# Kernel optimization log

Hardware: AMD Instinct MI355X
Metric: run time of the kernel (lower is better)

## Reference

```python
import jax, jax.numpy as jnp
import numpy as np

N_NODES = 50000
N_EDGES = 600000
IN_F = 128
OUT_F = 128
SMALL = max(IN_F // 10, 1)  # floor(128/10) = 12
D_K = np.sqrt(SMALL).astype(np.float32)


def setup_inputs() -> dict:
    key = jax.random.key(0)
    ks = jax.random.split(key, 10)
    node_data = jax.random.normal(ks[0], (N_NODES, IN_F), dtype=jnp.float32)
    src = jax.random.randint(ks[1], (N_EDGES,), 0, N_NODES, dtype=jnp.int32)
    dst = jax.random.randint(ks[2], (N_EDGES,), 0, N_NODES, dtype=jnp.int32)
    s_q = 1.0 / np.sqrt(IN_F)
    Wq = jax.random.uniform(ks[3], (SMALL, IN_F), jnp.float32, -s_q, s_q)
    bq = jax.random.uniform(ks[4], (SMALL,), jnp.float32, -s_q, s_q)
    Wk = jax.random.uniform(ks[5], (SMALL, IN_F), jnp.float32, -s_q, s_q)
    bk = jax.random.uniform(ks[6], (SMALL,), jnp.float32, -s_q, s_q)
    W1 = jax.random.uniform(ks[7], (OUT_F, IN_F), jnp.float32, -s_q, s_q)
    W2 = jax.random.uniform(ks[8], (OUT_F, IN_F), jnp.float32, -s_q, s_q)
    b2 = jax.random.uniform(ks[9], (OUT_F,), jnp.float32, -s_q, s_q)
    return {"node_data": node_data, "src": src, "dst": dst,
            "Wq": Wq, "bq": bq, "Wk": Wk, "bk": bk,
            "W1": W1, "W2": W2, "b2": b2}


def reference(node_data, src, dst, Wq, bq, Wk, bk, W1, W2, b2):
    N = node_data.shape[0]
    # dgl.add_self_loop: append (i, i) for every node -> each dst has >= 1 edge
    loops = jnp.arange(N, dtype=src.dtype)
    s = jnp.concatenate([src, loops])
    d = jnp.concatenate([dst, loops])

    # query = Tanh(Linear), key = Linear  (shapes [N, SMALL])
    q = jnp.tanh(node_data @ Wq.T + bq)
    k = node_data @ Wk.T + bk

    # per-edge score: sum(query[src] * key[dst]) / sqrt(small)
    scores = jnp.sum(q[s] * k[d], axis=1) / D_K  # [E]

    # softmax over incoming edges of each dst node (segment softmax)
    seg_max = jax.ops.segment_max(scores, d, num_segments=N)
    w = jnp.exp(scores - seg_max[d])
    seg_sum = jax.ops.segment_sum(w, d, num_segments=N)
    w = w / seg_sum[d]  # [E]

    # weighted scatter-aggregate of src node inputs -> [N, IN_F]
    att = jax.ops.segment_sum(w[:, None] * node_data[s], d, num_segments=N)

    # DeepSetLayer: layer1(node_data) + layer2(node attention)
    x = node_data @ W1.T + (att @ W2.T + b2)
    # per-row L2 ('fro' over dim=1) normalization, then ReLU
    x = x / jnp.linalg.norm(x, axis=1, keepdims=True)
    return jax.nn.relu(x)
```

## Files before the change

### kernel.cpp

```cpp
#include <hip/hip_runtime.h>
#include <hip/hip_bf16.h>
#include <math.h>
#include <stdint.h>


#define IN_F 128
#define SMALL 12
#define QK_PAD 16
#define SCAN_ITEMS 8
#define SCAN_CHUNK 2048

typedef __attribute__((ext_vector_type(8))) short short8;
typedef __attribute__((ext_vector_type(4))) float f32x4;

__device__ __forceinline__ unsigned short f2bf(float f) {
    union { float f; unsigned u; } v; v.f = f;
    unsigned r = v.u + 0x7fff + ((v.u >> 16) & 1);
    return (unsigned short)(r >> 16);
}

__device__ __forceinline__ float2 bf2x2(unsigned v) {
    union { unsigned u; float f; } a, b;
    a.u = v << 16;
    b.u = v & 0xffff0000u;
    return make_float2(a.f, b.f);
}

__device__ __forceinline__ float dot12(const float* __restrict__ qrow,
                                       float4 c0, float4 c1, float4 c2) {
    float4 a = ((const float4*)qrow)[0];
    float4 b = ((const float4*)qrow)[1];
    float4 c = ((const float4*)qrow)[2];
    return a.x*c0.x + a.y*c0.y + a.z*c0.z + a.w*c0.w
         + b.x*c1.x + b.y*c1.y + b.z*c1.z + b.w*c1.w
         + c.x*c2.x + c.y*c2.y + c.z*c2.z + c.w*c2.w;
}

__device__ __forceinline__ short8 ld_bf8(const float* p) {
    float4 x0 = *(const float4*)p;
    float4 x1 = *(const float4*)(p + 4);
    short8 a;
    a[0] = (short)f2bf(x0.x); a[1] = (short)f2bf(x0.y);
    a[2] = (short)f2bf(x0.z); a[3] = (short)f2bf(x0.w);
    a[4] = (short)f2bf(x1.x); a[5] = (short)f2bf(x1.y);
    a[6] = (short)f2bf(x1.z); a[7] = (short)f2bf(x1.w);
    return a;
}

__global__ __launch_bounds__(256) void prep_kernel(
    const float* __restrict__ nd,
    const float* __restrict__ Wq, const float* __restrict__ bq,
    const float* __restrict__ Wk, const float* __restrict__ bk,
    const int* __restrict__ dst,
    const float* __restrict__ W1, const float* __restrict__ W2,
    float* __restrict__ q, float* __restrict__ kf,
    unsigned short* __restrict__ ndb, int* __restrict__ cnt,
    unsigned short* __restrict__ rank, unsigned short* __restrict__ Wc,
    int N, int E, int NBQK, int NBCNT)
{
    int t = threadIdx.x;
    int b = blockIdx.x;

    if (b < NBQK) {
        int wv = t >> 6;
        int lane = t & 63;
        int col = lane & 15;
        int quad = lane >> 4;
        int tbase = b * 64 + wv * 16;

        int arow = tbase + col;
        int rowc = (arow < N) ? arow : (N - 1);
        const float* ap = nd + (size_t)rowc * IN_F + quad * 8;
        unsigned short* np = ndb + (size_t)arow * IN_F + quad * 8;

        const float* w0 = ((col < 12) ? (Wq + (size_t)col * IN_F)
                                      : (Wk + (size_t)(col - 12) * IN_F)) + quad * 8;
        const float* w1 = Wk + (size_t)((col < 8) ? (col + 4) : 4) * IN_F + quad * 8;
        bool hasw1 = (col < 8);

        f32x4 acc0 = (f32x4)0.f, acc1 = (f32x4)0.f;
#pragma unroll
        for (int ks = 0; ks < 4; ks++) {
            int k0 = ks * 32;
            short8 a = ld_bf8(ap + k0);
            if (arow < N) *(short8*)(np + k0) = a;
            short8 bb0 = ld_bf8(w0 + k0);
            short8 bb1 = hasw1 ? ld_bf8(w1 + k0) : (short8)0;
            acc0 = __builtin_amdgcn_mfma_f32_16x16x32_bf16(a, bb0, acc0, 0, 0, 0);
            acc1 = __builtin_amdgcn_mfma_f32_16x16x32_bf16(a, bb1, acc1, 0, 0, 0);
        }
        float bias0 = (col < 12) ? bq[col] : bk[col - 12];
        float bias1 = (col < 8) ? bk[col + 4] : 0.f;
#pragma unroll
        for (int r = 0; r < 4; r++) {
            int node = tbase + quad * 4 + r;
            if (node < N) {
                float v0 = acc0[r] + bias0;
                if (col < 12) q[(size_t)node * QK_PAD + col] = tanhf(v0);
                else          kf[(size_t)node * QK_PAD + (col - 12)] = v0;
                if (hasw1)    kf[(size_t)node * QK_PAD + col + 4] = acc1[r] + bias1;
            }
        }
    } else if (b < NBQK + NBCNT) {
        int ET = E + N;
        int stride = NBCNT * 256;
        for (int i = (b - NBQK) * 256 + t; i < ET; i += stride) {
            int d = (i < E) ? dst[i] : (i - E);
            rank[i] = (unsigned short)atomicAdd(&cnt[d], 1);
        }
    } else {
        int idx = (b - NBQK - NBCNT) * 256 + t;
        int f = idx >> 8, k = idx & 255;
        float v = (k < 128) ? W1[f * 128 + k] : W2[f * 128 + (k - 128)];
        Wc[idx] = f2bf(v);
    }
}

__global__ __launch_bounds__(256) void scan_local_kernel(
    int* __restrict__ off, int* __restrict__ bsum, int N)
{
    __shared__ int tsum[256];
    int t = threadIdx.x;
    int base = blockIdx.x * SCAN_CHUNK + t * SCAN_ITEMS;
    int v[SCAN_ITEMS];
    int s = 0;
#pragma unroll
    for (int i = 0; i < SCAN_ITEMS; i++) {
        int idx = base + i;
        v[i] = (idx < N) ? off[idx] : 0;
        s += v[i];
    }
    tsum[t] = s;
    __syncthreads();
    for (int d = 1; d < 256; d <<= 1) {
        int x = (t >= d) ? tsum[t - d] : 0;
        __syncthreads();
        tsum[t] += x;
        __syncthreads();
    }
    int excl = (t == 0) ? 0 : tsum[t - 1];
#pragma unroll
    for (int i = 0; i < SCAN_ITEMS; i++) {
        int idx = base + i;
        if (idx < N) off[idx] = excl;
        excl += v[i];
    }
    if (t == 255) bsum[blockIdx.x] = tsum[255];
}

__global__ __launch_bounds__(256) void scan_add_kernel(
    int* __restrict__ off, const int* __restrict__ bsum, int N, int NB)
{
    __shared__ int pre2[2];
    int t = threadIdx.x;
    if (t == 0) {
        int p = 0, tot = 0;
        for (int i = 0; i < NB; i++) {
            int v = bsum[i];
            if (i < (int)blockIdx.x) p += v;
            tot += v;
        }
        pre2[0] = p; pre2[1] = tot;
    }
    __syncthreads();
    int add = pre2[0];
    if (blockIdx.x == 0 && t == 0) off[N] = pre2[1];

    int base = blockIdx.x * SCAN_CHUNK + t * SCAN_ITEMS;
#pragma unroll
    for (int i = 0; i < SCAN_ITEMS; i++) {
        int j = base + i;
        if (j < N) off[j] += add;
    }
}

__global__ __launch_bounds__(256) void scatter_kernel(
    const int* __restrict__ src, const int* __restrict__ dst,
    const int* __restrict__ off, const unsigned short* __restrict__ rank,
    unsigned short* __restrict__ esrc, int E, int N)
{
    int i = blockIdx.x * 256 + threadIdx.x;
    if (i >= E + N) return;
    int d, s;
    if (i < E) { d = dst[i]; s = src[i]; }
    else       { d = i - E; s = d; }
    esrc[off[d] + (int)rank[i]] = (unsigned short)s;
}

__global__ __launch_bounds__(256) void attn_kernel(
    const unsigned short* __restrict__ ndb, const float* __restrict__ q,
    const float* __restrict__ kf, const int* __restrict__ off,
    const unsigned short* __restrict__ esrc, float* __restrict__ att, int N)
{
    const float INVDK = 0.28867513459481287f;
    int t = threadIdx.x;
    int lane = t & 63;
    int l16 = lane & 15;
    int gbase = lane & 48;
    int wid = blockIdx.x * 16 + (t >> 4);
    if (wid >= N) return;

    int start = off[wid];
    int deg = off[wid + 1] - start;

    const float4* kp = (const float4*)(kf + (size_t)wid * QK_PAD);
    float4 c0 = kp[0], c1 = kp[1], c2 = kp[2];

    float acc[8];
#pragma unroll
    for (int j = 0; j < 8; j++) acc[j] = 0.f;
    float inv;

    const unsigned short* nb = ndb + l16 * 8;

#define ACCUM(vv, ww) do {                                                    \
        float2 f0 = bf2x2((vv).x), f1 = bf2x2((vv).y);                        \
        float2 f2 = bf2x2((vv).z), f3 = bf2x2((vv).w);                        \
        acc[0] += (ww) * f0.x; acc[1] += (ww) * f0.y;                         \
        acc[2] += (ww) * f1.x; acc[3] += (ww) * f1.y;                         \
        acc[4] += (ww) * f2.x; acc[5] += (ww) * f2.y;                         \
        acc[6] += (ww) * f3.x; acc[7] += (ww) * f3.y;                         \
    } while (0)

    if (deg <= 16) {
        float sc = -INFINITY;
        int si = 0;
        if (l16 < deg) {
            si = (int)esrc[start + l16];
            sc = dot12(q + (size_t)si * QK_PAD, c0, c1, c2) * INVDK;
        }
        float m = sc;
#pragma unroll
        for (int o = 8; o > 0; o >>= 1) m = fmaxf(m, __shfl_xor(m, o));
        float w = (l16 < deg) ? __expf(sc - m) : 0.f;
        float ls = w;
#pragma unroll
        for (int o = 8; o > 0; o >>= 1) ls += __shfl_xor(ls, o);
        inv = 1.f / ls;

        int i = 0;
        for (; i + 4 <= deg; i += 4) {
            float w0 = __shfl(w, gbase | i);       int r0 = __shfl(si, gbase | i);
            float w1 = __shfl(w, gbase | (i + 1)); int r1 = __shfl(si, gbase | (i + 1));
            float w2 = __shfl(w, gbase | (i + 2)); int r2 = __shfl(si, gbase | (i + 2));
            float w3 = __shfl(w, gbase | (i + 3)); int r3 = __shfl(si, gbase | (i + 3));
            uint4 v0 = *(const uint4*)(nb + (size_t)r0 * IN_F);
            uint4 v1 = *(const uint4*)(nb + (size_t)r1 * IN_F);
            uint4 v2 = *(const uint4*)(nb + (size_t)r2 * IN_F);
            uint4 v3 = *(const uint4*)(nb + (size_t)r3 * IN_F);
            ACCUM(v0, w0); ACCUM(v1, w1); ACCUM(v2, w2); ACCUM(v3, w3);
        }
        for (; i < deg; i++) {
            float wi = __shfl(w, gbase | i);
            int ri = __shfl(si, gbase | i);
            uint4 v = *(const uint4*)(nb + (size_t)ri * IN_F);
            ACCUM(v, wi);
        }
    } else {
        float m = -INFINITY;
        for (int i = l16; i < deg; i += 16) {
            int s2 = (int)esrc[start + i];
            m = fmaxf(m, dot12(q + (size_t)s2 * QK_PAD, c0, c1, c2) * INVDK);
        }
#pragma unroll
        for (int o = 8; o > 0; o >>= 1) m = fmaxf(m, __shfl_xor(m, o));
        float ls = 0.f;
        for (int i = l16; i < deg; i += 16) {
            int s2 = (int)esrc[start + i];
            ls += __expf(dot12(q + (size_t)s2 * QK_PAD, c0, c1, c2) * INVDK - m);
        }
#pragma unroll
        for (int o = 8; o > 0; o >>= 1) ls += __shfl_xor(ls, o);
        inv = 1.f / ls;

        for (int base2 = 0; base2 < deg; base2 += 16) {
            int cnt2 = deg - base2; if (cnt2 > 16) cnt2 = 16;
            float w = 0.f; int si = 0;
            if (l16 < cnt2) {
                si = (int)esrc[start + base2 + l16];
                w = __expf(dot12(q + (size_t)si * QK_PAD, c0, c1, c2) * INVDK - m);
            }
            int i = 0;
            for (; i + 4 <= cnt2; i += 4) {
                float w0 = __shfl(w, gbase | i);       int r0 = __shfl(si, gbase | i);
                float w1 = __shfl(w, gbase | (i + 1)); int r1 = __shfl(si, gbase | (i + 1));
                float w2 = __shfl(w, gbase | (i + 2)); int r2 = __shfl(si, gbase | (i + 2));
                float w3 = __shfl(w, gbase | (i + 3)); int r3 = __shfl(si, gbase | (i + 3));
                uint4 v0 = *(const uint4*)(nb + (size_t)r0 * IN_F);
                uint4 v1 = *(const uint4*)(nb + (size_t)r1 * IN_F);
                uint4 v2 = *(const uint4*)(nb + (size_t)r2 * IN_F);
                uint4 v3 = *(const uint4*)(nb + (size_t)r3 * IN_F);
                ACCUM(v0, w0); ACCUM(v1, w1); ACCUM(v2, w2); ACCUM(v3, w3);
            }
            for (; i < cnt2; i++) {
                float wi = __shfl(w, gbase | i);
                int ri = __shfl(si, gbase | i);
                uint4 v = *(const uint4*)(nb + (size_t)ri * IN_F);
                ACCUM(v, wi);
            }
        }
    }
#undef ACCUM

    float* op = att + (size_t)wid * IN_F + l16 * 8;
    float4 s0, s1;
    s0.x = acc[0] * inv; s0.y = acc[1] * inv; s0.z = acc[2] * inv; s0.w = acc[3] * inv;
    s1.x = acc[4] * inv; s1.y = acc[5] * inv; s1.z = acc[6] * inv; s1.w = acc[7] * inv;
    *(float4*)op = s0;
    *(float4*)(op + 4) = s1;
}

__global__ __launch_bounds__(256) void final_kernel(
    const unsigned short* __restrict__ ndb, const float* __restrict__ nd,
    const float* __restrict__ att,
    const unsigned short* __restrict__ Wc, const float* __restrict__ b2,
    float* __restrict__ out, int N)
{
    int wv = threadIdx.x >> 6;
    int lane = threadIdx.x & 63;
    int col = lane & 15;
    int quad = lane >> 4;

    int arow = blockIdx.x * 64 + wv * 16 + col;
    int rowc = (arow < N) ? arow : (N - 1);
    const unsigned short* a0p = ndb + (size_t)rowc * IN_F + quad * 8;
    const float* a1p = ((arow < N) ? att : nd) + (size_t)rowc * IN_F + quad * 8;

    f32x4 acc[8];
#pragma unroll
    for (int i = 0; i < 8; i++) acc[i] = (f32x4)0.f;

#pragma unroll
    for (int ks = 0; ks < 8; ks++) {
        int k0 = ks * 32;
        short8 a;
        if (ks < 4) a = *(const short8*)(a0p + k0);
        else        a = ld_bf8(a1p + (k0 - 128));
#pragma unroll
        for (int ft = 0; ft < 8; ft++) {
            int n = ft * 16 + col;
            short8 bb = *(const short8*)(Wc + (size_t)n * 256 + k0 + quad * 8);
            acc[ft] = __builtin_amdgcn_mfma_f32_16x16x32_bf16(a, bb, acc[ft], 0, 0, 0);
        }
    }

    float bias[8];
#pragma unroll
    for (int ft = 0; ft < 8; ft++) bias[ft] = b2[ft * 16 + col];

#pragma unroll
    for (int r = 0; r < 4; r++) {
        int node = blockIdx.x * 64 + wv * 16 + quad * 4 + r;
        float v[8];
        float ps = 0.f;
#pragma unroll
        for (int ft = 0; ft < 8; ft++) {
            v[ft] = acc[ft][r] + bias[ft];
            ps += v[ft] * v[ft];
        }
        ps += __shfl_xor(ps, 1);
        ps += __shfl_xor(ps, 2);
        ps += __shfl_xor(ps, 4);
        ps += __shfl_xor(ps, 8);
        float rn = rsqrtf(ps);
        if (node < N) {
            float* op = out + (size_t)node * 128 + col;
#pragma unroll
            for (int ft = 0; ft < 8; ft++)
                op[ft * 16] = fmaxf(v[ft] * rn, 0.f);
        }
    }
}

static inline char* align_up(char* p, size_t a) {
    return (char*)(((uintptr_t)p + (a - 1)) & ~(uintptr_t)(a - 1));
}

extern "C" void kernel_launch(void* const* d_in, const int* in_sizes, int n_in,
                              void* d_out, int out_size, void* d_ws, size_t ws_size,
                              hipStream_t stream) {
    const float* node_data = (const float*)d_in[0];
    const int*   src       = (const int*)d_in[1];
    const int*   dst       = (const int*)d_in[2];
    const float* Wq        = (const float*)d_in[3];
    const float* bq        = (const float*)d_in[4];
    const float* Wk        = (const float*)d_in[5];
    const float* bk        = (const float*)d_in[6];
    const float* W1        = (const float*)d_in[7];
    const float* W2        = (const float*)d_in[8];
    const float* b2        = (const float*)d_in[9];
    float* out = (float*)d_out;

    int N = in_sizes[0] / IN_F;
    int E = in_sizes[1];
    int ET = E + N;
    int NB = (N + SCAN_CHUNK - 1) / SCAN_CHUNK;
    int NBQK = (N + 63) / 64;
    int NBCNT = 512;
    int NBCVT = 128;

    char* w = (char*)d_ws;
    float* q  = (float*)w;  w += (size_t)N * QK_PAD * sizeof(float);
    float* kf = (float*)w;  w += (size_t)N * QK_PAD * sizeof(float);
    w = align_up(w, 256);
    unsigned short* ndb = (unsigned short*)w;  w += (size_t)N * IN_F * sizeof(unsigned short);
    w = align_up(w, 256);
    unsigned short* Wc = (unsigned short*)w;  w += 128 * 256 * sizeof(unsigned short);
    int* off  = (int*)w;  w += (size_t)(N + 1) * sizeof(int);
    int* bsum = (int*)w;  w += 256 * sizeof(int);
    unsigned short* rank = (unsigned short*)w;  w += (size_t)ET * sizeof(unsigned short);
    w = align_up(w, 256);
    unsigned short* esrc = (unsigned short*)w;  w += (size_t)ET * sizeof(unsigned short);
    float* att = out;

    hipMemsetAsync(off, 0, (size_t)(N + 1) * sizeof(int), stream);

    prep_kernel<<<NBQK + NBCNT + NBCVT, 256, 0, stream>>>(
        node_data, Wq, bq, Wk, bk, dst, W1, W2,
        q, kf, ndb, off, rank, Wc, N, E, NBQK, NBCNT);
    scan_local_kernel<<<NB, 256, 0, stream>>>(off, bsum, N);
    scan_add_kernel<<<NB, 256, 0, stream>>>(off, bsum, N, NB);
    scatter_kernel<<<(ET + 255) / 256, 256, 0, stream>>>(src, dst, off, rank, esrc, E, N);
    attn_kernel<<<(N + 15) / 16, 256, 0, stream>>>(ndb, q, kf, off, esrc, att, N);
    final_kernel<<<(N + 63) / 64, 256, 0, stream>>>(ndb, node_data, att, Wc, b2, out, N);
}
```

Measured before the change: 221.9 us.

## Switch bf16 storage and MFMA to fp16 and prefetch first gathered rows

Replaces the bf16 software rounding and unpacking with native fp16 conversions across the prep, aggregation and final kernels, and uses fp16 MFMA in both matrix stages. For low-degree nodes, the first four neighbour rows are now gathered before the score, max and sum reductions so that load latency overlaps the softmax work. fp16 has less range than bf16, so large values could overflow. The prefetch also issues four loads even when degree is below four, reading node 0's row for the unused slots.

```diff
diff --git a/kernel.cpp b/kernel.cpp
--- a/kernel.cpp
+++ b/kernel.cpp
@@ -10,21 +10,8 @@
 #define SCAN_ITEMS 8
 #define SCAN_CHUNK 2048
 
-typedef __attribute__((ext_vector_type(8))) short short8;
+typedef __attribute__((ext_vector_type(8))) _Float16 half8;
 typedef __attribute__((ext_vector_type(4))) float f32x4;
-
-__device__ __forceinline__ unsigned short f2bf(float f) {
-    union { float f; unsigned u; } v; v.f = f;
-    unsigned r = v.u + 0x7fff + ((v.u >> 16) & 1);
-    return (unsigned short)(r >> 16);
-}
-
-__device__ __forceinline__ float2 bf2x2(unsigned v) {
-    union { unsigned u; float f; } a, b;
-    a.u = v << 16;
-    b.u = v & 0xffff0000u;
-    return make_float2(a.f, b.f);
-}
 
 __device__ __forceinline__ float dot12(const float* __restrict__ qrow,
                                        float4 c0, float4 c1, float4 c2) {
@@ -36,14 +23,14 @@
          + c.x*c2.x + c.y*c2.y + c.z*c2.z + c.w*c2.w;
 }
 
-__device__ __forceinline__ short8 ld_bf8(const float* p) {
+__device__ __forceinline__ half8 ld_h8(const float* p) {
     float4 x0 = *(const float4*)p;
     float4 x1 = *(const float4*)(p + 4);
-    short8 a;
-    a[0] = (short)f2bf(x0.x); a[1] = (short)f2bf(x0.y);
-    a[2] = (short)f2bf(x0.z); a[3] = (short)f2bf(x0.w);
-    a[4] = (short)f2bf(x1.x); a[5] = (short)f2bf(x1.y);
-    a[6] = (short)f2bf(x1.z); a[7] = (short)f2bf(x1.w);
+    half8 a;
+    a[0] = (_Float16)x0.x; a[1] = (_Float16)x0.y;
+    a[2] = (_Float16)x0.z; a[3] = (_Float16)x0.w;
+    a[4] = (_Float16)x1.x; a[5] = (_Float16)x1.y;
+    a[6] = (_Float16)x1.z; a[7] = (_Float16)x1.w;
     return a;
 }
 
@@ -78,16 +65,17 @@
         const float* w1 = Wk + (size_t)((col < 8) ? (col + 4) : 4) * IN_F + quad * 8;
         bool hasw1 = (col < 8);
 
+        half8 zero = {};
         f32x4 acc0 = (f32x4)0.f, acc1 = (f32x4)0.f;
 #pragma unroll
         for (int ks = 0; ks < 4; ks++) {
             int k0 = ks * 32;
-            short8 a = ld_bf8(ap + k0);
-            if (arow < N) *(short8*)(np + k0) = a;
-            short8 bb0 = ld_bf8(w0 + k0);
-            short8 bb1 = hasw1 ? ld_bf8(w1 + k0) : (short8)0;
-            acc0 = __builtin_amdgcn_mfma_f32_16x16x32_bf16(a, bb0, acc0, 0, 0, 0);
-            acc1 = __builtin_amdgcn_mfma_f32_16x16x32_bf16(a, bb1, acc1, 0, 0, 0);
+            half8 a = ld_h8(ap + k0);
+            if (arow < N) *(half8*)(np + k0) = a;
+            half8 bb0 = ld_h8(w0 + k0);
+            half8 bb1 = hasw1 ? ld_h8(w1 + k0) : zero;
+            acc0 = __builtin_amdgcn_mfma_f32_16x16x32_f16(a, bb0, acc0, 0, 0, 0);
+            acc1 = __builtin_amdgcn_mfma_f32_16x16x32_f16(a, bb1, acc1, 0, 0, 0);
         }
         float bias0 = (col < 12) ? bq[col] : bk[col - 12];
         float bias1 = (col < 8) ? bk[col + 4] : 0.f;
@@ -112,7 +100,7 @@
         int idx = (b - NBQK - NBCNT) * 256 + t;
         int f = idx >> 8, k = idx & 255;
         float v = (k < 128) ? W1[f * 128 + k] : W2[f * 128 + (k - 128)];
-        Wc[idx] = f2bf(v);
+        ((_Float16*)Wc)[idx] = (_Float16)v;
     }
 }
 
@@ -213,22 +201,29 @@
 
     const unsigned short* nb = ndb + l16 * 8;
 
-#define ACCUM(vv, ww) do {                                                    \
-        float2 f0 = bf2x2((vv).x), f1 = bf2x2((vv).y);                        \
-        float2 f2 = bf2x2((vv).z), f3 = bf2x2((vv).w);                        \
-        acc[0] += (ww) * f0.x; acc[1] += (ww) * f0.y;                         \
-        acc[2] += (ww) * f1.x; acc[3] += (ww) * f1.y;                         \
-        acc[4] += (ww) * f2.x; acc[5] += (ww) * f2.y;                         \
-        acc[6] += (ww) * f3.x; acc[7] += (ww) * f3.y;                         \
+#define ACCUM(hv, ww) do {                                                    \
+        acc[0] += (ww) * (float)(hv)[0]; acc[1] += (ww) * (float)(hv)[1];     \
+        acc[2] += (ww) * (float)(hv)[2]; acc[3] += (ww) * (float)(hv)[3];     \
+        acc[4] += (ww) * (float)(hv)[4]; acc[5] += (ww) * (float)(hv)[5];     \
+        acc[6] += (ww) * (float)(hv)[6]; acc[7] += (ww) * (float)(hv)[7];     \
     } while (0)
 
     if (deg <= 16) {
+        int si = 0;
+        if (l16 < deg) si = (int)esrc[start + l16];
+
+        int r0 = __shfl(si, gbase | 0);
+        int r1 = __shfl(si, gbase | 1);
+        int r2 = __shfl(si, gbase | 2);
+        int r3 = __shfl(si, gbase | 3);
+        half8 v0 = *(const half8*)(nb + (size_t)r0 * IN_F);
+        half8 v1 = *(const half8*)(nb + (size_t)r1 * IN_F);
+        half8 v2 = *(const half8*)(nb + (size_t)r2 * IN_F);
+        half8 v3 = *(const half8*)(nb + (size_t)r3 * IN_F);
+
         float sc = -INFINITY;
-        int si = 0;
-        if (l16 < deg) {
-            si = (int)esrc[start + l16];
+        if (l16 < deg)
             sc = dot12(q + (size_t)si * QK_PAD, c0, c1, c2) * INVDK;
-        }
         float m = sc;
 #pragma unroll
         for (int o = 8; o > 0; o >>= 1) m = fmaxf(m, __shfl_xor(m, o));
@@ -238,23 +233,29 @@
         for (int o = 8; o > 0; o >>= 1) ls += __shfl_xor(ls, o);
         inv = 1.f / ls;
 
-        int i = 0;
+        float w0 = __shfl(w, gbase | 0);
+        float w1 = __shfl(w, gbase | 1);
+        float w2 = __shfl(w, gbase | 2);
+        float w3 = __shfl(w, gbase | 3);
+        ACCUM(v0, w0); ACCUM(v1, w1); ACCUM(v2, w2); ACCUM(v3, w3);
+
+        int i = 4;
         for (; i + 4 <= deg; i += 4) {
-            float w0 = __shfl(w, gbase | i);       int r0 = __shfl(si, gbase | i);
-            float w1 = __shfl(w, gbase | (i + 1)); int r1 = __shfl(si, gbase | (i + 1));
-            float w2 = __shfl(w, gbase | (i + 2)); int r2 = __shfl(si, gbase | (i + 2));
-            float w3 = __shfl(w, gbase | (i + 3)); int r3 = __shfl(si, gbase | (i + 3));
-            uint4 v0 = *(const uint4*)(nb + (size_t)r0 * IN_F);
-            uint4 v1 = *(const uint4*)(nb + (size_t)r1 * IN_F);
-            uint4 v2 = *(const uint4*)(nb + (size_t)r2 * IN_F);
-            uint4 v3 = *(const uint4*)(nb + (size_t)r3 * IN_F);
-            ACCUM(v0, w0); ACCUM(v1, w1); ACCUM(v2, w2); ACCUM(v3, w3);
+            float u0 = __shfl(w, gbase | i);       int s0 = __shfl(si, gbase | i);
+            float u1 = __shfl(w, gbase | (i + 1)); int s1 = __shfl(si, gbase | (i + 1));
+            float u2 = __shfl(w, gbase | (i + 2)); int s2 = __shfl(si, gbase | (i + 2));
+            float u3 = __shfl(w, gbase | (i + 3)); int s3 = __shfl(si, gbase | (i + 3));
+            half8 x0 = *(const half8*)(nb + (size_t)s0 * IN_F);
+            half8 x1 = *(const half8*)(nb + (size_t)s1 * IN_F);
+            half8 x2 = *(const half8*)(nb + (size_t)s2 * IN_F);
+            half8 x3 = *(const half8*)(nb + (size_t)s3 * IN_F);
+            ACCUM(x0, u0); ACCUM(x1, u1); ACCUM(x2, u2); ACCUM(x3, u3);
         }
         for (; i < deg; i++) {
             float wi = __shfl(w, gbase | i);
             int ri = __shfl(si, gbase | i);
-            uint4 v = *(const uint4*)(nb + (size_t)ri * IN_F);
-            ACCUM(v, wi);
+            half8 x = *(const half8*)(nb + (size_t)ri * IN_F);
+            ACCUM(x, wi);
         }
     } else {
         float m = -INFINITY;
@@ -282,21 +283,21 @@
             }
             int i = 0;
             for (; i + 4 <= cnt2; i += 4) {
-                float w0 = __shfl(w, gbase | i);       int r0 = __shfl(si, gbase | i);
-                float w1 = __shfl(w, gbase | (i + 1)); int r1 = __shfl(si, gbase | (i + 1));
-                float w2 = __shfl(w, gbase | (i + 2)); int r2 = __shfl(si, gbase | (i + 2));
-                float w3 = __shfl(w, gbase | (i + 3)); int r3 = __shfl(si, gbase | (i + 3));
-                uint4 v0 = *(const uint4*)(nb + (size_t)r0 * IN_F);
-                uint4 v1 = *(const uint4*)(nb + (size_t)r1 * IN_F);
-                uint4 v2 = *(const uint4*)(nb + (size_t)r2 * IN_F);
-                uint4 v3 = *(const uint4*)(nb + (size_t)r3 * IN_F);
-                ACCUM(v0, w0); ACCUM(v1, w1); ACCUM(v2, w2); ACCUM(v3, w3);
+                float u0 = __shfl(w, gbase | i);       int s0 = __shfl(si, gbase | i);
+                float u1 = __shfl(w, gbase | (i + 1)); int s1 = __shfl(si, gbase | (i + 1));
+                float u2 = __shfl(w, gbase | (i + 2)); int s2 = __shfl(si, gbase | (i + 2));
+                float u3 = __shfl(w, gbase | (i + 3)); int s3 = __shfl(si, gbase | (i + 3));
+                half8 x0 = *(const half8*)(nb + (size_t)s0 * IN_F);
+                half8 x1 = *(const half8*)(nb + (size_t)s1 * IN_F);
+                half8 x2 = *(const half8*)(nb + (size_t)s2 * IN_F);
+                half8 x3 = *(const half8*)(nb + (size_t)s3 * IN_F);
+                ACCUM(x0, u0); ACCUM(x1, u1); ACCUM(x2, u2); ACCUM(x3, u3);
             }
             for (; i < cnt2; i++) {
                 float wi = __shfl(w, gbase | i);
                 int ri = __shfl(si, gbase | i);
-                uint4 v = *(const uint4*)(nb + (size_t)ri * IN_F);
-                ACCUM(v, wi);
+                half8 x = *(const half8*)(nb + (size_t)ri * IN_F);
+                ACCUM(x, wi);
             }
         }
     }
@@ -333,14 +334,14 @@
 #pragma unroll
     for (int ks = 0; ks < 8; ks++) {
         int k0 = ks * 32;
-        short8 a;
-        if (ks < 4) a = *(const short8*)(a0p + k0);
-        else        a = ld_bf8(a1p + (k0 - 128));
+        half8 a;
+        if (ks < 4) a = *(const half8*)(a0p + k0);
+        else        a = ld_h8(a1p + (k0 - 128));
 #pragma unroll
         for (int ft = 0; ft < 8; ft++) {
             int n = ft * 16 + col;
-            short8 bb = *(const short8*)(Wc + (size_t)n * 256 + k0 + quad * 8);
-            acc[ft] = __builtin_amdgcn_mfma_f32_16x16x32_bf16(a, bb, acc[ft], 0, 0, 0);
+            half8 bb = *(const half8*)(Wc + (size_t)n * 256 + k0 + quad * 8);
+            acc[ft] = __builtin_amdgcn_mfma_f32_16x16x32_f16(a, bb, acc[ft], 0, 0, 0);
         }
     }
 
```

Measured after the change: 221.5 us. About the same (-0.2%).
